# Performance work log

Hardware: AMD Instinct MI355X
Metric: run time of the kernel (lower is better)

The kernel has to match this reference:

```python
import jax, jax.numpy as jnp
import numpy as np
from jax import lax

REP_THR = 0.6
BORDER = 10


def setup_inputs() -> dict:
    key = jax.random.key(0)
    # repeatability heatmap in [0, 1), NCHW
    repeatability = jax.random.uniform(key, (16, 1, 1536, 1536), dtype=jnp.float32)
    return {"repeatability": repeatability}


def _local_max(x):
    # 3x3 stride-1 max pool with padding=1 (torch pads with -inf for maxpool)
    return lax.reduce_window(
        x, -jnp.inf, lax.max,
        window_dimensions=(1, 1, 3, 3),
        window_strides=(1, 1, 1, 1),
        padding=((0, 0), (0, 0), (1, 1), (1, 1)),
    )


def reference(repeatability):
    B, C, H, W = repeatability.shape
    maxima = (repeatability == _local_max(repeatability)) & (repeatability >= REP_THR)
    # border mask: zero out a 10-pixel frame
    border = jnp.zeros((H, W), dtype=bool).at[BORDER:-BORDER, BORDER:-BORDER].set(True)
    maxima = maxima & border  # broadcasts over (B, C)
    # nonzero().t()[2:4] -> row/col (y, x) coordinates of surviving maxima, shape [2, K]
    idx = jnp.nonzero(maxima)  # tuple (b, c, y, x); dynamic-shaped, eager only
    return jnp.stack(idx)[2:4]
```

## Files before the change

### kernel.cpp

```cpp
#include <hip/hip_runtime.h>

#define W 1536
#define H 1536
#define NB 16
#define NROWS (NB * H)
#define SH 32
#define NBLK1 (NROWS / SH)
#define BLOCK1 384
#define CPR 24
#define NMASK (NROWS * CPR)
#define BLOCK2 (SH * CPR)
#define REP_THR 0.6f

__device__ __forceinline__ float max3f(float a, float b, float c) {
    return fmaxf(fmaxf(a, b), c);
}

__device__ __forceinline__ float4 ld4u(const float* p) {
    float4 r;
    __builtin_memcpy(&r, p, 16);
    return r;
}

__global__ __launch_bounds__(BLOCK1) void nms_pass1(const float* __restrict__ in,
                                                    unsigned long long* __restrict__ masks,
                                                    unsigned int* __restrict__ counts) {
    const int t = threadIdx.x;
    const int lane = t & 63;
    const int wv = t >> 6;
    const int blk = blockIdx.x;
    const int r0 = blk * SH;
    const int ytile = blk % (H / SH);

    const int ca = (t == 0) ? 0 : 4 * t - 1;
    const int cb = (t == BLOCK1 - 1) ? 4 * t : 4 * t + 1;

    unsigned colm = 0xFu;
    if (t <= 1) colm = 0u;
    else if (t == 2) colm = 0xCu;
    if (t >= 382) colm = 0u;
    else if (t == 381) colm = 0x3u;

    auto rowp = [&](int i) {
        int ir = r0 - 1 + i;
        ir = ir < 0 ? 0 : (ir >= NROWS ? NROWS - 1 : ir);
        return in + (size_t)ir * W;
    };

    float4 va0 = ld4u(rowp(0) + ca), vb0 = ld4u(rowp(0) + cb);
    float4 va1 = ld4u(rowp(1) + ca), vb1 = ld4u(rowp(1) + cb);
    float4 vaN = ld4u(rowp(2) + ca), vbN = ld4u(rowp(2) + cb);

    float4 hA, hB, ctrB;
    hA.x = max3f(va0.x, va0.y, va0.z);
    hA.y = max3f(va0.y, va0.z, va0.w);
    hA.z = max3f(vb0.x, vb0.y, vb0.z);
    hA.w = max3f(vb0.y, vb0.z, vb0.w);
    hB.x = max3f(va1.x, va1.y, va1.z);
    hB.y = max3f(va1.y, va1.z, va1.w);
    hB.z = max3f(vb1.x, vb1.y, vb1.z);
    hB.w = max3f(vb1.y, vb1.z, vb1.w);
    ctrB.x = va1.y; ctrB.y = va1.z; ctrB.z = va1.w; ctrB.w = vb1.z;

    unsigned cnt = 0;
#pragma unroll
    for (int i = 2; i <= SH + 1; ++i) {
        float4 va = vaN, vb = vbN;
        vaN = ld4u(rowp(i + 1) + ca);
        vbN = ld4u(rowp(i + 1) + cb);
        float4 hC;
        hC.x = max3f(va.x, va.y, va.z);
        hC.y = max3f(va.y, va.z, va.w);
        hC.z = max3f(vb.x, vb.y, vb.z);
        hC.w = max3f(vb.y, vb.z, vb.w);

        const int yloc = ytile * SH + (i - 2);
        unsigned nib = 0u;
        if (yloc >= 10 && yloc < H - 10) {
            nib |= (ctrB.x >= fmaxf(max3f(hA.x, hB.x, hC.x), REP_THR)) ? 1u : 0u;
            nib |= (ctrB.y >= fmaxf(max3f(hA.y, hB.y, hC.y), REP_THR)) ? 2u : 0u;
            nib |= (ctrB.z >= fmaxf(max3f(hA.z, hB.z, hC.z), REP_THR)) ? 4u : 0u;
            nib |= (ctrB.w >= fmaxf(max3f(hA.w, hB.w, hC.w), REP_THR)) ? 8u : 0u;
            nib &= colm;
        }
        cnt += __popc(nib);
        unsigned x = nib;
        x |= __shfl_down(x, 1, 64) << 4;
        x |= __shfl_down(x, 2, 64) << 8;
        x |= __shfl_down(x, 4, 64) << 16;
        unsigned hi = __shfl_down(x, 8, 64);
        if ((lane & 15) == 0) {
            unsigned long long m64 = (unsigned long long)x | ((unsigned long long)hi << 32);
            masks[(size_t)(r0 + i - 2) * CPR + (t >> 4)] = m64;
        }
        hA = hB; hB = hC;
        ctrB.x = va.y; ctrB.y = va.z; ctrB.z = va.w; ctrB.w = vb.z;
    }

#pragma unroll
    for (int o = 32; o > 0; o >>= 1) cnt += __shfl_down(cnt, o, 64);
    __shared__ unsigned wsum[BLOCK1 / 64];
    if (lane == 0) wsum[wv] = cnt;
    __syncthreads();
    if (t == 0) {
        unsigned s = 0;
#pragma unroll
        for (int k = 0; k < BLOCK1 / 64; ++k) s += wsum[k];
        counts[blk] = s;
    }
}

__global__ __launch_bounds__(BLOCK2) void nms_scatter(const unsigned long long* __restrict__ masks,
                                                      const unsigned int* __restrict__ counts,
                                                      int* __restrict__ out, unsigned int K) {
    const int t = threadIdx.x, lane = t & 63, wv = t >> 6;
    const int blk = blockIdx.x;
    unsigned long long bits = masks[(size_t)blk * BLOCK2 + t];
    const unsigned cnt = (unsigned)__popcll(bits);
    unsigned incl = cnt;
#pragma unroll
    for (int o = 1; o < 64; o <<= 1) {
        unsigned u = __shfl_up(incl, o, 64);
        if (lane >= o) incl += u;
    }
    unsigned part = (t < blk) ? counts[t] : 0u;
#pragma unroll
    for (int o = 32; o > 0; o >>= 1) part += __shfl_down(part, o, 64);
    __shared__ unsigned wtot[BLOCK2 / 64];
    __shared__ unsigned coff[BLOCK2 / 64];
    if (lane == 63) wtot[wv] = incl;
    if (lane == 0) coff[wv] = part;
    __syncthreads();
    unsigned pos = incl - cnt;
#pragma unroll
    for (int k = 0; k < BLOCK2 / 64; ++k) {
        pos += coff[k];
        pos += (k < wv) ? wtot[k] : 0u;
    }
    if (bits) {
        const int y = (blk % (H / SH)) * SH + t / CPR;
        const int x0 = (t % CPR) * 64;
        while (bits) {
            int j = __builtin_ctzll(bits);
            bits &= bits - 1ull;
            if (pos < K) { out[pos] = y; out[K + pos] = x0 + j; }
            ++pos;
        }
    }
}

extern "C" void kernel_launch(void* const* d_in, const int* in_sizes, int n_in,
                              void* d_out, int out_size, void* d_ws, size_t ws_size,
                              hipStream_t stream) {
    const float* in = (const float*)d_in[0];
    int* out = (int*)d_out;
    unsigned long long* masks = (unsigned long long*)d_ws;
    unsigned int* counts = (unsigned int*)((char*)d_ws + (size_t)NMASK * 8);
    const unsigned K = (unsigned)(out_size / 2);

    nms_pass1<<<NBLK1, BLOCK1, 0, stream>>>(in, masks, counts);
    nms_scatter<<<NBLK1, BLOCK2, 0, stream>>>(masks, counts, out, K);
}
```

Baseline: 252.2 us.

## Fuse mask pass and scatter into one cooperative kernel with grid sync

Merges the two kernels into a single cooperative launch. Per-block bitmasks now stay in LDS instead of going through global memory, and a grid-wide sync separates the counting phase from the prefix-sum and scatter phase. The tile height grows from 32 to 48 rows so that 512 blocks fit co-resident (3 per CU), which removes the second launch and the global mask round trip. In exchange it adds a grid barrier and a larger serial per-thread scatter loop, and it relies on every block being resident at once.

```diff
diff --git a/kernel.cpp b/kernel.cpp
--- a/kernel.cpp
+++ b/kernel.cpp
@@ -1,15 +1,18 @@
 #include <hip/hip_runtime.h>
+#include <hip/hip_cooperative_groups.h>
+
+namespace cg = cooperative_groups;
 
 #define W 1536
 #define H 1536
 #define NB 16
 #define NROWS (NB * H)
-#define SH 32
-#define NBLK1 (NROWS / SH)
-#define BLOCK1 384
+#define SH 48
+#define NBLK (NROWS / SH)
+#define BLOCK 384
 #define CPR 24
-#define NMASK (NROWS * CPR)
-#define BLOCK2 (SH * CPR)
+#define CHUNKS (SH * CPR)
+#define CPT (CHUNKS / BLOCK)
 #define REP_THR 0.6f
 
 __device__ __forceinline__ float max3f(float a, float b, float c) {
@@ -22,9 +25,14 @@
     return r;
 }
 
-__global__ __launch_bounds__(BLOCK1) void nms_pass1(const float* __restrict__ in,
-                                                    unsigned long long* __restrict__ masks,
-                                                    unsigned int* __restrict__ counts) {
+__global__ __launch_bounds__(BLOCK, 3) void nms_fused(const float* __restrict__ in,
+                                                      unsigned int* __restrict__ counts,
+                                                      int* __restrict__ out,
+                                                      unsigned int K) {
+    __shared__ unsigned long long lmask[CHUNKS];
+    __shared__ unsigned wred[BLOCK / 64];
+    __shared__ unsigned sred[BLOCK / 64];
+
     const int t = threadIdx.x;
     const int lane = t & 63;
     const int wv = t >> 6;
@@ -33,7 +41,7 @@
     const int ytile = blk % (H / SH);
 
     const int ca = (t == 0) ? 0 : 4 * t - 1;
-    const int cb = (t == BLOCK1 - 1) ? 4 * t : 4 * t + 1;
+    const int cb = (t == BLOCK - 1) ? 4 * t : 4 * t + 1;
 
     unsigned colm = 0xFu;
     if (t <= 1) colm = 0u;
@@ -63,7 +71,7 @@
     ctrB.x = va1.y; ctrB.y = va1.z; ctrB.z = va1.w; ctrB.w = vb1.z;
 
     unsigned cnt = 0;
-#pragma unroll
+#pragma unroll 8
     for (int i = 2; i <= SH + 1; ++i) {
         float4 va = vaN, vb = vbN;
         vaN = ld4u(rowp(i + 1) + ca);
@@ -91,7 +99,7 @@
         unsigned hi = __shfl_down(x, 8, 64);
         if ((lane & 15) == 0) {
             unsigned long long m64 = (unsigned long long)x | ((unsigned long long)hi << 32);
-            masks[(size_t)(r0 + i - 2) * CPR + (t >> 4)] = m64;
+            lmask[(i - 2) * CPR + (t >> 4)] = m64;
         }
         hA = hB; hB = hC;
         ctrB.x = va.y; ctrB.y = va.z; ctrB.z = va.w; ctrB.w = vb.z;
@@ -99,52 +107,59 @@
 
 #pragma unroll
     for (int o = 32; o > 0; o >>= 1) cnt += __shfl_down(cnt, o, 64);
-    __shared__ unsigned wsum[BLOCK1 / 64];
-    if (lane == 0) wsum[wv] = cnt;
+    if (lane == 0) wred[wv] = cnt;
     __syncthreads();
     if (t == 0) {
         unsigned s = 0;
 #pragma unroll
-        for (int k = 0; k < BLOCK1 / 64; ++k) s += wsum[k];
-        counts[blk] = s;
+        for (int k = 0; k < BLOCK / 64; ++k) s += wred[k];
+        __hip_atomic_store(&counts[blk], s, __ATOMIC_RELEASE, __HIP_MEMORY_SCOPE_AGENT);
     }
-}
 
-__global__ __launch_bounds__(BLOCK2) void nms_scatter(const unsigned long long* __restrict__ masks,
-                                                      const unsigned int* __restrict__ counts,
-                                                      int* __restrict__ out, unsigned int K) {
-    const int t = threadIdx.x, lane = t & 63, wv = t >> 6;
-    const int blk = blockIdx.x;
-    unsigned long long bits = masks[(size_t)blk * BLOCK2 + t];
-    const unsigned cnt = (unsigned)__popcll(bits);
-    unsigned incl = cnt;
+    cg::this_grid().sync();
+
+    unsigned long long b[CPT];
+    unsigned c[CPT];
+    unsigned cnt2 = 0;
+#pragma unroll
+    for (int k = 0; k < CPT; ++k) {
+        b[k] = lmask[t * CPT + k];
+        c[k] = (unsigned)__popcll(b[k]);
+        cnt2 += c[k];
+    }
+    unsigned incl = cnt2;
 #pragma unroll
     for (int o = 1; o < 64; o <<= 1) {
         unsigned u = __shfl_up(incl, o, 64);
         if (lane >= o) incl += u;
     }
-    unsigned part = (t < blk) ? counts[t] : 0u;
+    unsigned part = 0;
+    if (t < blk) part += __hip_atomic_load(&counts[t], __ATOMIC_ACQUIRE, __HIP_MEMORY_SCOPE_AGENT);
+    if (t + BLOCK < blk) part += __hip_atomic_load(&counts[t + BLOCK], __ATOMIC_ACQUIRE, __HIP_MEMORY_SCOPE_AGENT);
 #pragma unroll
     for (int o = 32; o > 0; o >>= 1) part += __shfl_down(part, o, 64);
-    __shared__ unsigned wtot[BLOCK2 / 64];
-    __shared__ unsigned coff[BLOCK2 / 64];
-    if (lane == 63) wtot[wv] = incl;
-    if (lane == 0) coff[wv] = part;
+    if (lane == 63) wred[wv] = incl;
+    if (lane == 0) sred[wv] = part;
     __syncthreads();
-    unsigned pos = incl - cnt;
+    unsigned pos = incl - cnt2;
 #pragma unroll
-    for (int k = 0; k < BLOCK2 / 64; ++k) {
-        pos += coff[k];
-        pos += (k < wv) ? wtot[k] : 0u;
+    for (int k = 0; k < BLOCK / 64; ++k) {
+        pos += sred[k];
+        if (k < wv) pos += wred[k];
     }
-    if (bits) {
-        const int y = (blk % (H / SH)) * SH + t / CPR;
-        const int x0 = (t % CPR) * 64;
-        while (bits) {
-            int j = __builtin_ctzll(bits);
-            bits &= bits - 1ull;
-            if (pos < K) { out[pos] = y; out[K + pos] = x0 + j; }
-            ++pos;
+#pragma unroll
+    for (int k = 0; k < CPT; ++k) {
+        unsigned long long bits = b[k];
+        if (bits) {
+            const int cidx = t * CPT + k;
+            const int y = ytile * SH + cidx / CPR;
+            const int x0 = (cidx % CPR) * 64;
+            while (bits) {
+                int j = __builtin_ctzll(bits);
+                bits &= bits - 1ull;
+                if (pos < K) { out[pos] = y; out[K + pos] = x0 + j; }
+                ++pos;
+            }
         }
     }
 }
@@ -154,10 +169,9 @@
                               hipStream_t stream) {
     const float* in = (const float*)d_in[0];
     int* out = (int*)d_out;
-    unsigned long long* masks = (unsigned long long*)d_ws;
-    unsigned int* counts = (unsigned int*)((char*)d_ws + (size_t)NMASK * 8);
-    const unsigned K = (unsigned)(out_size / 2);
+    unsigned int* counts = (unsigned int*)d_ws;
+    unsigned int K = (unsigned int)(out_size / 2);
 
-    nms_pass1<<<NBLK1, BLOCK1, 0, stream>>>(in, masks, counts);
-    nms_scatter<<<NBLK1, BLOCK2, 0, stream>>>(masks, counts, out, K);
+    void* args[] = {(void*)&in, (void*)&counts, (void*)&out, (void*)&K};
+    hipLaunchCooperativeKernel((void*)nms_fused, dim3(NBLK), dim3(BLOCK), args, 0, stream);
 }
```

Result: slower. 356.1 us (+41.2%).

## Use aligned loads with shuffle halos, halve pass1 rows, stage scatter output in LDS

Applied to the files above, without the earlier changes.

Pass 1 now does one aligned float4 load per thread per row and gets the left and right neighbours through wave shuffles, instead of two overlapping unaligned float4 loads. Only the edge lanes do extra scalar loads. Rows per block drop to 16, which doubles the pass-1 grid, so scatter now sums two counts per block when computing its prefix. Scatter packs coordinates into shared memory and writes them out coalesced, falling back to direct scattered writes when a block has more than CAP points. The costs are extra shuffles, a larger prefix read and 24KB of LDS per scatter block.

```diff
diff --git a/kernel.cpp b/kernel.cpp
--- a/kernel.cpp
+++ b/kernel.cpp
@@ -4,22 +4,19 @@
 #define H 1536
 #define NB 16
 #define NROWS (NB * H)
-#define SH 32
-#define NBLK1 (NROWS / SH)
+#define SH1 16
+#define NBLK1 (NROWS / SH1)
 #define BLOCK1 384
 #define CPR 24
 #define NMASK (NROWS * CPR)
-#define BLOCK2 (SH * CPR)
+#define SH2 32
+#define NBLK2 (NROWS / SH2)
+#define BLOCK2 (SH2 * CPR)
+#define CAP 6144
 #define REP_THR 0.6f
 
 __device__ __forceinline__ float max3f(float a, float b, float c) {
     return fmaxf(fmaxf(a, b), c);
-}
-
-__device__ __forceinline__ float4 ld4u(const float* p) {
-    float4 r;
-    __builtin_memcpy(&r, p, 16);
-    return r;
 }
 
 __global__ __launch_bounds__(BLOCK1) void nms_pass1(const float* __restrict__ in,
@@ -29,11 +26,12 @@
     const int lane = t & 63;
     const int wv = t >> 6;
     const int blk = blockIdx.x;
-    const int r0 = blk * SH;
-    const int ytile = blk % (H / SH);
+    const int r0 = blk * SH1;
+    const int ytile = blk % (H / SH1);
 
-    const int ca = (t == 0) ? 0 : 4 * t - 1;
-    const int cb = (t == BLOCK1 - 1) ? 4 * t : 4 * t + 1;
+    const int c0 = 4 * t;
+    const int cl = (t == 0) ? 0 : c0 - 1;
+    const int cr = (t == BLOCK1 - 1) ? (W - 1) : c0 + 4;
 
     unsigned colm = 0xFu;
     if (t <= 1) colm = 0u;
@@ -47,34 +45,49 @@
         return in + (size_t)ir * W;
     };
 
-    float4 va0 = ld4u(rowp(0) + ca), vb0 = ld4u(rowp(0) + cb);
-    float4 va1 = ld4u(rowp(1) + ca), vb1 = ld4u(rowp(1) + cb);
-    float4 vaN = ld4u(rowp(2) + ca), vbN = ld4u(rowp(2) + cb);
+    auto mkhalo = [&](float4 v, float lw, float rx) {
+        float lw_all = __shfl_up(v.w, 1, 64);
+        if (lane == 0) lw_all = lw;
+        float rx_all = __shfl_down(v.x, 1, 64);
+        if (lane == 63) rx_all = rx;
+        float4 h;
+        h.x = max3f(lw_all, v.x, v.y);
+        h.y = max3f(v.x, v.y, v.z);
+        h.z = max3f(v.y, v.z, v.w);
+        h.w = max3f(v.z, v.w, rx_all);
+        return h;
+    };
 
-    float4 hA, hB, ctrB;
-    hA.x = max3f(va0.x, va0.y, va0.z);
-    hA.y = max3f(va0.y, va0.z, va0.w);
-    hA.z = max3f(vb0.x, vb0.y, vb0.z);
-    hA.w = max3f(vb0.y, vb0.z, vb0.w);
-    hB.x = max3f(va1.x, va1.y, va1.z);
-    hB.y = max3f(va1.y, va1.z, va1.w);
-    hB.z = max3f(vb1.x, vb1.y, vb1.z);
-    hB.w = max3f(vb1.y, vb1.z, vb1.w);
-    ctrB.x = va1.y; ctrB.y = va1.z; ctrB.z = va1.w; ctrB.w = vb1.z;
+    float4 v0 = *(const float4*)(rowp(0) + c0);
+    float lw0 = 0.f, rx0 = 0.f;
+    if (lane == 0) lw0 = rowp(0)[cl];
+    if (lane == 63) rx0 = rowp(0)[cr];
+    float4 v1 = *(const float4*)(rowp(1) + c0);
+    float lw1 = 0.f, rx1 = 0.f;
+    if (lane == 0) lw1 = rowp(1)[cl];
+    if (lane == 63) rx1 = rowp(1)[cr];
+    float4 vN = *(const float4*)(rowp(2) + c0);
+    float lwN = 0.f, rxN = 0.f;
+    if (lane == 0) lwN = rowp(2)[cl];
+    if (lane == 63) rxN = rowp(2)[cr];
+
+    float4 hA = mkhalo(v0, lw0, rx0);
+    float4 hB = mkhalo(v1, lw1, rx1);
+    float4 ctrB = v1;
 
     unsigned cnt = 0;
 #pragma unroll
-    for (int i = 2; i <= SH + 1; ++i) {
-        float4 va = vaN, vb = vbN;
-        vaN = ld4u(rowp(i + 1) + ca);
-        vbN = ld4u(rowp(i + 1) + cb);
-        float4 hC;
-        hC.x = max3f(va.x, va.y, va.z);
-        hC.y = max3f(va.y, va.z, va.w);
-        hC.z = max3f(vb.x, vb.y, vb.z);
-        hC.w = max3f(vb.y, vb.z, vb.w);
+    for (int i = 2; i <= SH1 + 1; ++i) {
+        float4 v = vN;
+        float lwc = lwN, rxc = rxN;
+        vN = *(const float4*)(rowp(i + 1) + c0);
+        lwN = 0.f; rxN = 0.f;
+        if (lane == 0) lwN = rowp(i + 1)[cl];
+        if (lane == 63) rxN = rowp(i + 1)[cr];
 
-        const int yloc = ytile * SH + (i - 2);
+        float4 hC = mkhalo(v, lwc, rxc);
+
+        const int yloc = ytile * SH1 + (i - 2);
         unsigned nib = 0u;
         if (yloc >= 10 && yloc < H - 10) {
             nib |= (ctrB.x >= fmaxf(max3f(hA.x, hB.x, hC.x), REP_THR)) ? 1u : 0u;
@@ -93,8 +106,7 @@
             unsigned long long m64 = (unsigned long long)x | ((unsigned long long)hi << 32);
             masks[(size_t)(r0 + i - 2) * CPR + (t >> 4)] = m64;
         }
-        hA = hB; hB = hC;
-        ctrB.x = va.y; ctrB.y = va.z; ctrB.z = va.w; ctrB.w = vb.z;
+        hA = hB; hB = hC; ctrB = v;
     }
 
 #pragma unroll
@@ -113,6 +125,9 @@
 __global__ __launch_bounds__(BLOCK2) void nms_scatter(const unsigned long long* __restrict__ masks,
                                                       const unsigned int* __restrict__ counts,
                                                       int* __restrict__ out, unsigned int K) {
+    __shared__ unsigned wtot[BLOCK2 / 64];
+    __shared__ unsigned sred[BLOCK2 / 64];
+    __shared__ unsigned pk[CAP];
     const int t = threadIdx.x, lane = t & 63, wv = t >> 6;
     const int blk = blockIdx.x;
     unsigned long long bits = masks[(size_t)blk * BLOCK2 + t];
@@ -123,28 +138,45 @@
         unsigned u = __shfl_up(incl, o, 64);
         if (lane >= o) incl += u;
     }
-    unsigned part = (t < blk) ? counts[t] : 0u;
+    unsigned part = 0;
+    if (t < 2 * blk) part += counts[t];
+    if (t + BLOCK2 < 2 * blk) part += counts[t + BLOCK2];
 #pragma unroll
     for (int o = 32; o > 0; o >>= 1) part += __shfl_down(part, o, 64);
-    __shared__ unsigned wtot[BLOCK2 / 64];
-    __shared__ unsigned coff[BLOCK2 / 64];
     if (lane == 63) wtot[wv] = incl;
-    if (lane == 0) coff[wv] = part;
+    if (lane == 0) sred[wv] = part;
     __syncthreads();
-    unsigned pos = incl - cnt;
+    unsigned blockBase = 0, blockCnt = 0, wbase = 0;
 #pragma unroll
     for (int k = 0; k < BLOCK2 / 64; ++k) {
-        pos += coff[k];
-        pos += (k < wv) ? wtot[k] : 0u;
+        blockBase += sred[k];
+        blockCnt += wtot[k];
+        if (k < wv) wbase += wtot[k];
     }
+    unsigned local = wbase + (incl - cnt);
     if (bits) {
-        const int y = (blk % (H / SH)) * SH + t / CPR;
+        const int y = (blk % (H / SH2)) * SH2 + t / CPR;
         const int x0 = (t % CPR) * 64;
         while (bits) {
             int j = __builtin_ctzll(bits);
             bits &= bits - 1ull;
-            if (pos < K) { out[pos] = y; out[K + pos] = x0 + j; }
-            ++pos;
+            if (local < CAP) {
+                pk[local] = (unsigned)y | ((unsigned)(x0 + j) << 16);
+            } else {
+                unsigned g = blockBase + local;
+                if (g < K) { out[g] = y; out[K + g] = x0 + j; }
+            }
+            ++local;
+        }
+    }
+    __syncthreads();
+    const unsigned lim = blockCnt < CAP ? blockCnt : CAP;
+    for (unsigned i = t; i < lim; i += BLOCK2) {
+        unsigned g = blockBase + i;
+        if (g < K) {
+            unsigned p = pk[i];
+            out[g] = (int)(p & 0xFFFFu);
+            out[K + g] = (int)(p >> 16);
         }
     }
 }
@@ -159,5 +191,5 @@
     const unsigned K = (unsigned)(out_size / 2);
 
     nms_pass1<<<NBLK1, BLOCK1, 0, stream>>>(in, masks, counts);
-    nms_scatter<<<NBLK1, BLOCK2, 0, stream>>>(masks, counts, out, K);
+    nms_scatter<<<NBLK2, BLOCK2, 0, stream>>>(masks, counts, out, K);
 }
```

New measurement: 234.8 us. 6.9% less time.
